# Performance work log

Hardware: AMD Instinct MI355X
Metric: run time of the kernel (lower is better)

## Reference

```python
import jax, jax.numpy as jnp
import numpy as np

H = 8  # number of heads


def setup_inputs() -> dict:
    key = jax.random.key(0)
    ks = jax.random.split(key, 7)
    B, L, D = 4, 2048, 512
    dh = D // H
    s = 1.0 / np.sqrt(D).astype(np.float32)
    return {
        "q": jax.random.normal(ks[0], (B, L, D), jnp.float32),
        "k": jax.random.normal(ks[1], (B, L, D), jnp.float32),
        "v": jax.random.normal(ks[2], (B, L, D), jnp.float32),
        "Wq": jax.random.normal(ks[3], (D, D), jnp.float32) * s,
        "Wk": jax.random.normal(ks[4], (D, D), jnp.float32) * s,
        "Wv": jax.random.normal(ks[5], (D, D), jnp.float32) * s,
        "E": jax.random.normal(ks[6], (L, dh), jnp.float32) * s,
    }


def _skew(QE):
    # QE: [B, H, L, L] -> pad one column on the left, reshape to [B,H,L+1,L],
    # drop the first row: the classic Music Transformer skewing trick.
    B, h, L, M = QE.shape
    padded = jnp.pad(QE, ((0, 0), (0, 0), (0, 0), (1, 0)))
    return padded.reshape(B, h, M + 1, L)[:, :, 1:, :]


def reference(q, k, v, Wq, Wk, Wv, E):
    B, L, D = q.shape
    dh = D // H

    def heads(x, W):
        return jnp.einsum('bld,de->ble', x, W).reshape(B, L, H, dh).transpose(0, 2, 1, 3)

    qh = heads(q, Wq)  # [B,H,L,dh]
    kh = heads(k, Wk)
    vh = heads(v, Wv)

    QE = jnp.einsum('bhld,md->bhlm', qh, E)      # [B,H,L,L]
    Srel = _skew(QE)                             # [B,H,L,L]
    QKt = jnp.einsum('bhld,bhmd->bhlm', qh, kh)  # [B,H,L,L]

    # NOTE: original divides AFTER softmax (faithful to source).
    attn = jax.nn.softmax(QKt + Srel, axis=-1) / float(np.sqrt(dh))
    out = jnp.einsum('bhlm,bhmd->bhld', attn, vh)
    return out.transpose(0, 2, 1, 3).reshape(B, L, D)
```

## Files before the change

kernel.cpp:

```cpp
#include <hip/hip_runtime.h>
#include <hip/hip_bf16.h>
#include <math.h>

typedef _Float16 f16;
typedef __attribute__((ext_vector_type(8))) _Float16 f16x8;
typedef __attribute__((ext_vector_type(4))) _Float16 f16x4;
typedef __attribute__((ext_vector_type(4))) float f32x4;

namespace {
constexpr int B = 4, L = 2048, D = 512, NH = 8, DH = 64;
}

__global__ __launch_bounds__(256)
void ecast_kernel(const float* __restrict__ E, f16* __restrict__ Ef) {
    int i4 = (blockIdx.x * 256 + threadIdx.x) * 4;
    float4 x = *(const float4*)(E + i4);
    *(f16x4*)(Ef + i4) = (f16x4){(f16)x.x, (f16)x.y, (f16)x.z, (f16)x.w};
}

__global__ __launch_bounds__(256)
void wtrans_kernel(const float* __restrict__ Wq, const float* __restrict__ Wk,
                   const float* __restrict__ Wv, f16* __restrict__ Wt) {
    __shared__ f16 Ws[64 * 65];
    const int sel = blockIdx.z;
    const float* W = (sel == 0) ? Wq : (sel == 1) ? Wk : Wv;
    f16* Wo = Wt + (size_t)sel * D * D;
    const int k0 = blockIdx.x * 64, n0 = blockIdx.y * 64;
    const int t = threadIdx.x;
#pragma unroll
    for (int i = 0; i < 16; ++i) {
        int idx = 256 * i + t;
        int r = idx >> 6, c = idx & 63;
        Ws[r * 65 + c] = (f16)W[(size_t)(k0 + r) * D + n0 + c];
    }
    __syncthreads();
    const int c = t >> 2, kseg = t & 3;
    f16x8 r0, r1;
#pragma unroll
    for (int j = 0; j < 8; ++j) r0[j] = Ws[(kseg * 16 + j) * 65 + c];
#pragma unroll
    for (int j = 0; j < 8; ++j) r1[j] = Ws[(kseg * 16 + 8 + j) * 65 + c];
    f16* o = Wo + (size_t)(n0 + c) * D + k0 + kseg * 16;
    *(f16x8*)o = r0;
    *(f16x8*)(o + 8) = r1;
}

__global__ __launch_bounds__(256, 4)
void proj_gemm(const float* __restrict__ q, const float* __restrict__ k,
               const float* __restrict__ v, const f16* __restrict__ Wt,
               f16* __restrict__ Qf, f16* __restrict__ Kf, f16* __restrict__ Vtf) {
    __shared__ f16 As[128 * 72];
    __shared__ f16 Bs[64 * 72];
    const int bx = blockIdx.x, by = blockIdx.y;
    const int sel = by >> 3, h = by & 7;
    const int m0 = bx * 128;
    const float* X = (sel == 0) ? q : (sel == 1) ? k : v;
    const f16* Bt = Wt + (size_t)sel * D * D + (size_t)h * 64 * D;
    const int t = threadIdx.x, wid = t >> 6, lane = t & 63;
    const int quad = lane >> 4, col = lane & 15;
    const int mw = wid * 32;

    f32x4 acc[2][4];
#pragma unroll
    for (int i = 0; i < 2; ++i)
#pragma unroll
        for (int j = 0; j < 4; ++j) acc[i][j] = (f32x4){0.f, 0.f, 0.f, 0.f};

    float4 xa[8];
    f16x8 breg[2];
    auto loadG = [&](int k0) {
#pragma unroll
        for (int i = 0; i < 8; ++i) {
            int idx = 256 * i + t;
            int r = idx >> 4, c4 = idx & 15;
            xa[i] = *(const float4*)(X + (size_t)(m0 + r) * D + k0 + c4 * 4);
        }
#pragma unroll
        for (int i = 0; i < 2; ++i) {
            int idx = 256 * i + t;
            int r = idx >> 3, ch = idx & 7;
            breg[i] = *(const f16x8*)(Bt + (size_t)r * D + k0 + ch * 8);
        }
    };
    auto storeL = [&]() {
#pragma unroll
        for (int i = 0; i < 8; ++i) {
            int idx = 256 * i + t;
            int r = idx >> 4, c4 = idx & 15;
            *(f16x4*)(As + r * 72 + c4 * 4) =
                (f16x4){(f16)xa[i].x, (f16)xa[i].y, (f16)xa[i].z, (f16)xa[i].w};
        }
#pragma unroll
        for (int i = 0; i < 2; ++i) {
            int idx = 256 * i + t;
            int r = idx >> 3, ch = idx & 7;
            *(f16x8*)(Bs + r * 72 + ch * 8) = breg[i];
        }
    };

    loadG(0);
    for (int k0 = 0; k0 < D; k0 += 64) {
        __syncthreads();
        storeL();
        __syncthreads();
        if (k0 + 64 < D) loadG(k0 + 64);
#pragma unroll
        for (int ks = 0; ks < 2; ++ks) {
            f16x8 af[2], bf[4];
#pragma unroll
            for (int mt = 0; mt < 2; ++mt)
                af[mt] = *(const f16x8*)(As + (mw + mt * 16 + col) * 72 + quad * 8 + ks * 32);
#pragma unroll
            for (int nt = 0; nt < 4; ++nt)
                bf[nt] = *(const f16x8*)(Bs + (nt * 16 + col) * 72 + quad * 8 + ks * 32);
#pragma unroll
            for (int mt = 0; mt < 2; ++mt)
#pragma unroll
                for (int nt = 0; nt < 4; ++nt)
                    acc[mt][nt] = __builtin_amdgcn_mfma_f32_16x16x32_f16(af[mt], bf[nt], acc[mt][nt], 0, 0, 0);
        }
    }

    if (sel < 2) {
        f16* Y = (sel == 0) ? Qf : Kf;
#pragma unroll
        for (int mt = 0; mt < 2; ++mt)
#pragma unroll
            for (int nt = 0; nt < 4; ++nt)
#pragma unroll
                for (int reg = 0; reg < 4; ++reg) {
                    int m = m0 + mw + mt * 16 + quad * 4 + reg;
                    int bb = m >> 11, l = m & 2047, d = nt * 16 + col;
                    Y[((size_t)(bb * NH + h) * L + l) * DH + d] = (f16)acc[mt][nt][reg];
                }
    } else {
        __syncthreads();
        f16* Cs = As;
#pragma unroll
        for (int mt = 0; mt < 2; ++mt)
#pragma unroll
            for (int nt = 0; nt < 4; ++nt)
#pragma unroll
                for (int reg = 0; reg < 4; ++reg) {
                    int d = nt * 16 + col;
                    int lc = mw + mt * 16 + quad * 4 + reg;
                    Cs[d * 136 + lc] = (f16)acc[mt][nt][reg];
                }
        __syncthreads();
        const int dd = t >> 2, seg = t & 3;
        const int bb = m0 >> 11, l0 = m0 & 2047;
        f16* Yv = Vtf + ((size_t)(bb * NH + h) * DH + dd) * L + l0 + seg * 32;
#pragma unroll
        for (int j = 0; j < 4; ++j)
            *(f16x8*)(Yv + j * 8) = *(const f16x8*)(Cs + dd * 136 + seg * 32 + j * 8);
    }
}

__global__ __launch_bounds__(256, 4)
void attn_kernel(const f16* __restrict__ Qf, const f16* __restrict__ Kf,
                 const f16* __restrict__ Vtf, const f16* __restrict__ Ef,
                 float* __restrict__ out) {
    __shared__ f16 KfS[64 * 72];
    __shared__ f16 VfS[64 * 72];
    __shared__ f16 Pbuf[4][16 * 72];

    const int t = threadIdx.x, wid = t >> 6, lane = t & 63;
    const int quad = lane >> 4, col = lane & 15;
    const int l0w = blockIdx.x * 64 + wid * 16;
    const int h = blockIdx.y, bb = blockIdx.z;
    const size_t head = (size_t)(bb * NH + h) * (size_t)(L * DH);
    const f16* qf = Qf + head;
    const f16* kf = Kf + head;
    const f16* vt = Vtf + head;
    f16* Pw = Pbuf[wid];

    f16x8 qF[2], qS[2];
    {
        const int m = l0w + col;
        const int mS = min(m + 1, L - 1);
#pragma unroll
        for (int ks = 0; ks < 2; ++ks) {
            const int off = quad * 8 + ks * 32;
            qF[ks] = *(const f16x8*)(qf + (size_t)m * DH + off);
            qS[ks] = *(const f16x8*)(qf + (size_t)mS * DH + off);
        }
    }

    f16x8 kreg[2], vreg[2];
    auto loadKV = [&](int c0) {
#pragma unroll
        for (int i = 0; i < 2; ++i) {
            int idx = 256 * i + t;
            int r = idx >> 3, ch = idx & 7;
            kreg[i] = *(const f16x8*)(kf + (size_t)(c0 + r) * DH + ch * 8);
            vreg[i] = *(const f16x8*)(vt + (size_t)r * L + c0 + ch * 8);
        }
    };

    f32x4 O[4];
#pragma unroll
    for (int i = 0; i < 4; ++i) O[i] = (f32x4){0.f, 0.f, 0.f, 0.f};
    float mrow[4] = {-1e30f, -1e30f, -1e30f, -1e30f};
    float srow[4] = {0.f, 0.f, 0.f, 0.f};

    loadKV(0);
    for (int c0 = 0; c0 < L; c0 += 64) {
        __syncthreads();
#pragma unroll
        for (int i = 0; i < 2; ++i) {
            int idx = 256 * i + t;
            int r = idx >> 3, ch = idx & 7;
            *(f16x8*)(KfS + r * 72 + ch * 8) = kreg[i];
            *(f16x8*)(VfS + r * 72 + ch * 8) = vreg[i];
        }
        __syncthreads();
        if (c0 + 64 < L) loadKV(c0 + 64);

        const int d0 = c0 - l0w;

        f32x4 S[4];
#pragma unroll
        for (int ns = 0; ns < 4; ++ns) {
            S[ns] = (f32x4){0.f, 0.f, 0.f, 0.f};
#pragma unroll
            for (int ks = 0; ks < 2; ++ks) {
                f16x8 bh = *(const f16x8*)(KfS + (ns * 16 + col) * 72 + quad * 8 + ks * 32);
                S[ns] = __builtin_amdgcn_mfma_f32_16x16x32_f16(qF[ks], bh, S[ns], 0, 0, 0);
            }
        }

        const bool doA = (d0 <= 15);
        const bool doB = (d0 >= -61);
#pragma unroll 1
        for (int pass = 0; pass < 2; ++pass) {
            if ((pass == 0 && !doA) || (pass == 1 && !doB)) continue;
            const int jbase = (pass == 0) ? (d0 + L - 16) : (d0 - 17);
            f32x4 G[5];
#pragma unroll
            for (int g = 0; g < 5; ++g) {
                int er = min(max(jbase + g * 16 + col, 0), L - 1);
                G[g] = (f32x4){0.f, 0.f, 0.f, 0.f};
                const size_t eb = (size_t)er * DH + quad * 8;
#pragma unroll
                for (int ks = 0; ks < 2; ++ks) {
                    f16x8 e8 = *(const f16x8*)(Ef + eb + ks * 32);
                    G[g] = __builtin_amdgcn_mfma_f32_16x16x32_f16(
                               (pass == 0) ? qF[ks] : qS[ks], e8, G[g], 0, 0, 0);
                }
            }
#pragma unroll
            for (int reg = 0; reg < 4; ++reg) {
                const int r  = quad * 4 + reg;
                const int jj = col - r + 15;
                const int src = quad * 16 + (jj & 15);
#pragma unroll
                for (int ns = 0; ns < 4; ++ns) {
                    float v0 = __shfl(G[ns][reg], src, 64);
                    float v1 = __shfl(G[ns + 1][reg], src, 64);
                    float val = (jj < 16) ? v0 : v1;
                    const int rel = d0 + ns * 16 + col - r;
                    const bool use = (pass == 0) ? (rel <= 0) : (rel >= 2);
                    if (use) S[ns][reg] += val;
                }
            }
        }

#pragma unroll
        for (int reg = 0; reg < 4; ++reg) {
            float tm = fmaxf(fmaxf(S[0][reg], S[1][reg]), fmaxf(S[2][reg], S[3][reg]));
#pragma unroll
            for (int msk = 1; msk < 16; msk <<= 1)
                tm = fmaxf(tm, __shfl_xor(tm, msk, 16));
            const float mnew  = fmaxf(mrow[reg], tm);
            const float alpha = __expf(mrow[reg] - mnew);
            float p[4], ps = 0.f;
#pragma unroll
            for (int ns = 0; ns < 4; ++ns) { p[ns] = __expf(S[ns][reg] - mnew); ps += p[ns]; }
#pragma unroll
            for (int msk = 1; msk < 16; msk <<= 1)
                ps += __shfl_xor(ps, msk, 16);
            srow[reg] = srow[reg] * alpha + ps;
            mrow[reg] = mnew;
            const int r = quad * 4 + reg;
#pragma unroll
            for (int ns = 0; ns < 4; ++ns) {
                O[ns][reg] *= alpha;
                Pw[r * 72 + ns * 16 + col] = (f16)p[ns];
            }
        }

        f16x8 pA[2];
        pA[0] = *(const f16x8*)(Pw + col * 72 + quad * 8);
        pA[1] = *(const f16x8*)(Pw + col * 72 + 32 + quad * 8);
#pragma unroll
        for (int ns = 0; ns < 4; ++ns) {
#pragma unroll
            for (int ks = 0; ks < 2; ++ks) {
                f16x8 v8 = *(const f16x8*)(VfS + (ns * 16 + col) * 72 + quad * 8 + ks * 32);
                O[ns] = __builtin_amdgcn_mfma_f32_16x16x32_f16(pA[ks], v8, O[ns], 0, 0, 0);
            }
        }
    }

#pragma unroll
    for (int reg = 0; reg < 4; ++reg) {
        const int l = l0w + quad * 4 + reg;
        const float inv = 1.0f / (srow[reg] * 8.0f);
        float* o = out + ((size_t)bb * L + l) * D + h * DH;
#pragma unroll
        for (int ns = 0; ns < 4; ++ns)
            o[ns * 16 + col] = O[ns][reg] * inv;
    }
}

extern "C" void kernel_launch(void* const* d_in, const int* in_sizes, int n_in,
                              void* d_out, int out_size, void* d_ws, size_t ws_size,
                              hipStream_t stream) {
    const float* q  = (const float*)d_in[0];
    const float* k  = (const float*)d_in[1];
    const float* v  = (const float*)d_in[2];
    const float* Wq = (const float*)d_in[3];
    const float* Wk = (const float*)d_in[4];
    const float* Wv = (const float*)d_in[5];
    const float* E  = (const float*)d_in[6];
    float* out = (float*)d_out;

    const size_t plane = (size_t)B * NH * L * DH;
    f16* Qf  = (f16*)d_ws;
    f16* Kfp = Qf + plane;
    f16* Vtf = Kfp + plane;
    f16* Wt  = Vtf + plane;
    f16* Ef  = Wt + (size_t)3 * D * D;

    ecast_kernel<<<L * DH / 1024, 256, 0, stream>>>(E, Ef);
    wtrans_kernel<<<dim3(8, 8, 3), 256, 0, stream>>>(Wq, Wk, Wv, Wt);
    proj_gemm<<<dim3(64, 24), 256, 0, stream>>>(q, k, v, Wt, Qf, Kfp, Vtf);
    attn_kernel<<<dim3(L / 64, NH, B), 256, 0, stream>>>(Qf, Kfp, Vtf, Ef, out);
}
```

Measured before the change: 354.8 us.

## Split attention over key range, swizzle LDS tiles, remap projection block order

Attention now splits the key dimension in two (flash-decoding style), writing unnormalized partial outputs and row max/sum stats that a new combine kernel merges. This doubles the number of workgroups (1024 to 2048) to fill more CUs. K/V shared tiles drop padding in favour of an XOR swizzle to avoid LDS bank conflicts. Projection GEMM blocks are remapped so that neighbouring blocks land on different XCDs. The split adds extra fp32 partial writes and reads plus a kernel launch, and it only runs when the workspace is large enough.

```diff
diff --git a/kernel.cpp b/kernel.cpp
--- a/kernel.cpp
+++ b/kernel.cpp
@@ -51,7 +51,9 @@
                f16* __restrict__ Qf, f16* __restrict__ Kf, f16* __restrict__ Vtf) {
     __shared__ f16 As[128 * 72];
     __shared__ f16 Bs[64 * 72];
-    const int bx = blockIdx.x, by = blockIdx.y;
+    const int flat = blockIdx.x;
+    const int wg = (flat & 7) * 192 + (flat >> 3);
+    const int by = wg % 24, bx = wg / 24;
     const int sel = by >> 3, h = by & 7;
     const int m0 = bx * 128;
     const float* X = (sel == 0) ? q : (sel == 1) ? k : v;
@@ -156,23 +158,30 @@
     }
 }
 
+template <int NS>
 __global__ __launch_bounds__(256, 4)
 void attn_kernel(const f16* __restrict__ Qf, const f16* __restrict__ Kf,
                  const f16* __restrict__ Vtf, const f16* __restrict__ Ef,
-                 float* __restrict__ out) {
-    __shared__ f16 KfS[64 * 72];
-    __shared__ f16 VfS[64 * 72];
-    __shared__ f16 Pbuf[4][16 * 72];
+                 float* __restrict__ out, float* __restrict__ Opart,
+                 float2* __restrict__ stats) {
+    __shared__ __align__(16) f16 KfS[64 * 64];
+    __shared__ __align__(16) f16 VfS[64 * 64];
+    __shared__ __align__(16) f16 Pbuf[4][16 * 72];
 
     const int t = threadIdx.x, wid = t >> 6, lane = t & 63;
     const int quad = lane >> 4, col = lane & 15;
     const int l0w = blockIdx.x * 64 + wid * 16;
-    const int h = blockIdx.y, bb = blockIdx.z;
+    const int h = blockIdx.y;
+    const int bz = blockIdx.z;
+    const int bb = (NS == 1) ? bz : (bz >> 1);
+    const int split = (NS == 1) ? 0 : (bz & 1);
+    const int cbeg = split * (L / NS), cend = cbeg + L / NS;
     const size_t head = (size_t)(bb * NH + h) * (size_t)(L * DH);
     const f16* qf = Qf + head;
     const f16* kf = Kf + head;
     const f16* vt = Vtf + head;
     f16* Pw = Pbuf[wid];
+    const int rsw = col & 7;
 
     f16x8 qF[2], qS[2];
     {
@@ -203,18 +212,19 @@
     float mrow[4] = {-1e30f, -1e30f, -1e30f, -1e30f};
     float srow[4] = {0.f, 0.f, 0.f, 0.f};
 
-    loadKV(0);
-    for (int c0 = 0; c0 < L; c0 += 64) {
+    loadKV(cbeg);
+    for (int c0 = cbeg; c0 < cend; c0 += 64) {
         __syncthreads();
 #pragma unroll
         for (int i = 0; i < 2; ++i) {
             int idx = 256 * i + t;
             int r = idx >> 3, ch = idx & 7;
-            *(f16x8*)(KfS + r * 72 + ch * 8) = kreg[i];
-            *(f16x8*)(VfS + r * 72 + ch * 8) = vreg[i];
-        }
-        __syncthreads();
-        if (c0 + 64 < L) loadKV(c0 + 64);
+            int sw = ((ch ^ (r & 7)) << 3);
+            *(f16x8*)(KfS + r * 64 + sw) = kreg[i];
+            *(f16x8*)(VfS + r * 64 + sw) = vreg[i];
+        }
+        __syncthreads();
+        if (c0 + 64 < cend) loadKV(c0 + 64);
 
         const int d0 = c0 - l0w;
 
@@ -224,7 +234,8 @@
             S[ns] = (f32x4){0.f, 0.f, 0.f, 0.f};
 #pragma unroll
             for (int ks = 0; ks < 2; ++ks) {
-                f16x8 bh = *(const f16x8*)(KfS + (ns * 16 + col) * 72 + quad * 8 + ks * 32);
+                f16x8 bh = *(const f16x8*)(KfS + (ns * 16 + col) * 64 +
+                                           (((quad + ks * 4) ^ rsw) << 3));
                 S[ns] = __builtin_amdgcn_mfma_f32_16x16x32_f16(qF[ks], bh, S[ns], 0, 0, 0);
             }
         }
@@ -296,21 +307,61 @@
         for (int ns = 0; ns < 4; ++ns) {
 #pragma unroll
             for (int ks = 0; ks < 2; ++ks) {
-                f16x8 v8 = *(const f16x8*)(VfS + (ns * 16 + col) * 72 + quad * 8 + ks * 32);
+                f16x8 v8 = *(const f16x8*)(VfS + (ns * 16 + col) * 64 +
+                                           (((quad + ks * 4) ^ rsw) << 3));
                 O[ns] = __builtin_amdgcn_mfma_f32_16x16x32_f16(pA[ks], v8, O[ns], 0, 0, 0);
             }
         }
     }
 
-#pragma unroll
-    for (int reg = 0; reg < 4; ++reg) {
-        const int l = l0w + quad * 4 + reg;
-        const float inv = 1.0f / (srow[reg] * 8.0f);
-        float* o = out + ((size_t)bb * L + l) * D + h * DH;
-#pragma unroll
-        for (int ns = 0; ns < 4; ++ns)
-            o[ns * 16 + col] = O[ns][reg] * inv;
-    }
+    if (NS == 1) {
+#pragma unroll
+        for (int reg = 0; reg < 4; ++reg) {
+            const int l = l0w + quad * 4 + reg;
+            const float inv = 1.0f / (srow[reg] * 8.0f);
+            float* o = out + ((size_t)bb * L + l) * D + h * DH;
+#pragma unroll
+            for (int ns = 0; ns < 4; ++ns)
+                o[ns * 16 + col] = O[ns][reg] * inv;
+        }
+    } else {
+#pragma unroll
+        for (int reg = 0; reg < 4; ++reg) {
+            const int l = l0w + quad * 4 + reg;
+            const size_t rowid = ((size_t)(split * B + bb) * NH + h) * L + l;
+            float* op = Opart + rowid * DH;
+#pragma unroll
+            for (int ns = 0; ns < 4; ++ns)
+                op[ns * 16 + col] = O[ns][reg];
+            if (col == 0) stats[rowid] = make_float2(mrow[reg], srow[reg]);
+        }
+    }
+}
+
+__global__ __launch_bounds__(256)
+void combine_kernel(const float* __restrict__ Opart, const float2* __restrict__ stats,
+                    float* __restrict__ out) {
+    constexpr size_t OPLANE = (size_t)B * NH * L * DH;
+    constexpr int SROWS = B * NH * L;
+    const int gid = blockIdx.x * 256 + threadIdx.x;
+    const int d4 = gid & 15;
+    const int row = gid >> 4;
+    const float2 s0 = stats[row];
+    const float2 s1 = stats[SROWS + row];
+    const float M = fmaxf(s0.x, s1.x);
+    const float w0 = __expf(s0.x - M), w1 = __expf(s1.x - M);
+    const float inv = 1.0f / ((w0 * s0.y + w1 * s1.y) * 8.0f);
+    const float4 o0 = *(const float4*)(Opart + (size_t)row * DH + d4 * 4);
+    const float4 o1 = *(const float4*)(Opart + OPLANE + (size_t)row * DH + d4 * 4);
+    const int l = row & (L - 1);
+    const int bh = row >> 11;
+    const int hh = bh & 7, bbb = bh >> 3;
+    float4 r;
+    r.x = (w0 * o0.x + w1 * o1.x) * inv;
+    r.y = (w0 * o0.y + w1 * o1.y) * inv;
+    r.z = (w0 * o0.z + w1 * o1.z) * inv;
+    r.w = (w0 * o0.w + w1 * o1.w) * inv;
+    *(float4*)(out + ((size_t)bbb * L + l) * D + hh * DH + d4 * 4) = r;
 }
 
 extern "C" void kernel_launch(void* const* d_in, const int* in_sizes, int n_in,
@@ -331,9 +382,22 @@
     f16* Vtf = Kfp + plane;
     f16* Wt  = Vtf + plane;
     f16* Ef  = Wt + (size_t)3 * D * D;
+    const size_t base_bytes = (3 * plane + 3 * (size_t)D * D + (size_t)L * DH) * sizeof(f16);
+    float*  Opart = (float*)((char*)d_ws + base_bytes);
+    float2* stats = (float2*)((char*)d_ws + base_bytes + 2 * plane * sizeof(float));
+    const size_t need = base_bytes + 2 * plane * sizeof(float)
+                        + (size_t)2 * B * NH * L * sizeof(float2);
+    const bool split2 = (ws_size >= need);
 
     ecast_kernel<<<L * DH / 1024, 256, 0, stream>>>(E, Ef);
     wtrans_kernel<<<dim3(8, 8, 3), 256, 0, stream>>>(Wq, Wk, Wv, Wt);
-    proj_gemm<<<dim3(64, 24), 256, 0, stream>>>(q, k, v, Wt, Qf, Kfp, Vtf);
-    attn_kernel<<<dim3(L / 64, NH, B), 256, 0, stream>>>(Qf, Kfp, Vtf, Ef, out);
-}
+    proj_gemm<<<dim3(1536), 256, 0, stream>>>(q, k, v, Wt, Qf, Kfp, Vtf);
+    if (split2) {
+        attn_kernel<2><<<dim3(L / 64, NH, B * 2), 256, 0, stream>>>(Qf, Kfp, Vtf, Ef,
+                                                                    out, Opart, stats);
+        combine_kernel<<<(B * NH * L * 16) / 256, 256, 0, stream>>>(Opart, stats, out);
+    } else {
+        attn_kernel<1><<<dim3(L / 64, NH, B), 256, 0, stream>>>(Qf, Kfp, Vtf, Ef,
+                                                                out, Opart, stats);
+    }
+}
```

After: 392.4 us. 1.11x slower.

## Precast inputs to fp16, remap projection blocks, and compute softmax row sums via MFMA

Applied to the files above, without the earlier changes.

Adds a separate kernel that casts q/k/v to fp16 once, so the projection GEMM reads half the bytes per tile. The GEMM now uses a flat grid with a swizzled block order to group tiles across XCDs. In attention, the per-row softmax sum is computed with an MFMA against a ones vector instead of shuffle reductions, the first two max-reduction steps use DPP, and s_setprio is raised around the MFMA sections. The cost is an extra kernel launch plus a full fp16 copy of the inputs written to and read back from memory, and the row sum is now taken over fp16-rounded probabilities.

```diff
diff --git a/kernel.cpp b/kernel.cpp
--- a/kernel.cpp
+++ b/kernel.cpp
@@ -9,6 +9,13 @@
 
 namespace {
 constexpr int B = 4, L = 2048, D = 512, NH = 8, DH = 64;
+}
+
+__device__ __forceinline__ float dpp_xor1(float x) {
+    return __int_as_float(__builtin_amdgcn_update_dpp(0, __float_as_int(x), 0xB1, 0xF, 0xF, true));
+}
+__device__ __forceinline__ float dpp_xor2(float x) {
+    return __int_as_float(__builtin_amdgcn_update_dpp(0, __float_as_int(x), 0x4E, 0xF, 0xF, true));
 }
 
 __global__ __launch_bounds__(256)
@@ -16,6 +23,17 @@
     int i4 = (blockIdx.x * 256 + threadIdx.x) * 4;
     float4 x = *(const float4*)(E + i4);
     *(f16x4*)(Ef + i4) = (f16x4){(f16)x.x, (f16)x.y, (f16)x.z, (f16)x.w};
+}
+
+__global__ __launch_bounds__(256)
+void xcast_kernel(const float* __restrict__ q, const float* __restrict__ k,
+                  const float* __restrict__ v, f16* __restrict__ Xf) {
+    const int sel = blockIdx.y;
+    const float* X = (sel == 0) ? q : (sel == 1) ? k : v;
+    const size_t i4 = ((size_t)blockIdx.x * 256 + threadIdx.x) * 4;
+    float4 x = *(const float4*)(X + i4);
+    *(f16x4*)(Xf + (size_t)sel * ((size_t)B * L * D) + i4) =
+        (f16x4){(f16)x.x, (f16)x.y, (f16)x.z, (f16)x.w};
 }
 
 __global__ __launch_bounds__(256)
@@ -46,15 +64,16 @@
 }
 
 __global__ __launch_bounds__(256, 4)
-void proj_gemm(const float* __restrict__ q, const float* __restrict__ k,
-               const float* __restrict__ v, const f16* __restrict__ Wt,
+void proj_gemm(const f16* __restrict__ Xf, const f16* __restrict__ Wt,
                f16* __restrict__ Qf, f16* __restrict__ Kf, f16* __restrict__ Vtf) {
     __shared__ f16 As[128 * 72];
     __shared__ f16 Bs[64 * 72];
-    const int bx = blockIdx.x, by = blockIdx.y;
+    const int flat = blockIdx.x;
+    const int wg = (flat & 7) * 192 + (flat >> 3);
+    const int by = wg % 24, bx = wg / 24;
     const int sel = by >> 3, h = by & 7;
     const int m0 = bx * 128;
-    const float* X = (sel == 0) ? q : (sel == 1) ? k : v;
+    const f16* X = Xf + (size_t)sel * ((size_t)B * L * D);
     const f16* Bt = Wt + (size_t)sel * D * D + (size_t)h * 64 * D;
     const int t = threadIdx.x, wid = t >> 6, lane = t & 63;
     const int quad = lane >> 4, col = lane & 15;
@@ -66,14 +85,14 @@
 #pragma unroll
         for (int j = 0; j < 4; ++j) acc[i][j] = (f32x4){0.f, 0.f, 0.f, 0.f};
 
-    float4 xa[8];
+    f16x8 xa[4];
     f16x8 breg[2];
     auto loadG = [&](int k0) {
 #pragma unroll
-        for (int i = 0; i < 8; ++i) {
-            int idx = 256 * i + t;
-            int r = idx >> 4, c4 = idx & 15;
-            xa[i] = *(const float4*)(X + (size_t)(m0 + r) * D + k0 + c4 * 4);
+        for (int i = 0; i < 4; ++i) {
+            int idx = 256 * i + t;
+            int r = idx >> 3, ch = idx & 7;
+            xa[i] = *(const f16x8*)(X + (size_t)(m0 + r) * D + k0 + ch * 8);
         }
 #pragma unroll
         for (int i = 0; i < 2; ++i) {
@@ -84,11 +103,10 @@
     };
     auto storeL = [&]() {
 #pragma unroll
-        for (int i = 0; i < 8; ++i) {
-            int idx = 256 * i + t;
-            int r = idx >> 4, c4 = idx & 15;
-            *(f16x4*)(As + r * 72 + c4 * 4) =
-                (f16x4){(f16)xa[i].x, (f16)xa[i].y, (f16)xa[i].z, (f16)xa[i].w};
+        for (int i = 0; i < 4; ++i) {
+            int idx = 256 * i + t;
+            int r = idx >> 3, ch = idx & 7;
+            *(f16x8*)(As + r * 72 + ch * 8) = xa[i];
         }
 #pragma unroll
         for (int i = 0; i < 2; ++i) {
@@ -174,6 +192,9 @@
     const f16* vt = Vtf + head;
     f16* Pw = Pbuf[wid];
 
+    const f16x8 ones8 = {(f16)1.f, (f16)1.f, (f16)1.f, (f16)1.f,
+                         (f16)1.f, (f16)1.f, (f16)1.f, (f16)1.f};
+
     f16x8 qF[2], qS[2];
     {
         const int m = l0w + col;
@@ -200,8 +221,8 @@
     f32x4 O[4];
 #pragma unroll
     for (int i = 0; i < 4; ++i) O[i] = (f32x4){0.f, 0.f, 0.f, 0.f};
+    f32x4 sacc = (f32x4){0.f, 0.f, 0.f, 0.f};
     float mrow[4] = {-1e30f, -1e30f, -1e30f, -1e30f};
-    float srow[4] = {0.f, 0.f, 0.f, 0.f};
 
     loadKV(0);
     for (int c0 = 0; c0 < L; c0 += 64) {
@@ -219,6 +240,7 @@
         const int d0 = c0 - l0w;
 
         f32x4 S[4];
+        __builtin_amdgcn_s_setprio(1);
 #pragma unroll
         for (int ns = 0; ns < 4; ++ns) {
             S[ns] = (f32x4){0.f, 0.f, 0.f, 0.f};
@@ -228,6 +250,7 @@
                 S[ns] = __builtin_amdgcn_mfma_f32_16x16x32_f16(qF[ks], bh, S[ns], 0, 0, 0);
             }
         }
+        __builtin_amdgcn_s_setprio(0);
 
         const bool doA = (d0 <= 15);
         const bool doB = (d0 >= -61);
@@ -268,30 +291,29 @@
 #pragma unroll
         for (int reg = 0; reg < 4; ++reg) {
             float tm = fmaxf(fmaxf(S[0][reg], S[1][reg]), fmaxf(S[2][reg], S[3][reg]));
-#pragma unroll
-            for (int msk = 1; msk < 16; msk <<= 1)
-                tm = fmaxf(tm, __shfl_xor(tm, msk, 16));
+            tm = fmaxf(tm, dpp_xor1(tm));
+            tm = fmaxf(tm, dpp_xor2(tm));
+            tm = fmaxf(tm, __shfl_xor(tm, 4, 16));
+            tm = fmaxf(tm, __shfl_xor(tm, 8, 16));
             const float mnew  = fmaxf(mrow[reg], tm);
             const float alpha = __expf(mrow[reg] - mnew);
-            float p[4], ps = 0.f;
-#pragma unroll
-            for (int ns = 0; ns < 4; ++ns) { p[ns] = __expf(S[ns][reg] - mnew); ps += p[ns]; }
-#pragma unroll
-            for (int msk = 1; msk < 16; msk <<= 1)
-                ps += __shfl_xor(ps, msk, 16);
-            srow[reg] = srow[reg] * alpha + ps;
             mrow[reg] = mnew;
+            sacc[reg] *= alpha;
             const int r = quad * 4 + reg;
 #pragma unroll
             for (int ns = 0; ns < 4; ++ns) {
+                float p = __expf(S[ns][reg] - mnew);
                 O[ns][reg] *= alpha;
-                Pw[r * 72 + ns * 16 + col] = (f16)p[ns];
+                Pw[r * 72 + ns * 16 + col] = (f16)p;
             }
         }
 
         f16x8 pA[2];
         pA[0] = *(const f16x8*)(Pw + col * 72 + quad * 8);
         pA[1] = *(const f16x8*)(Pw + col * 72 + 32 + quad * 8);
+        __builtin_amdgcn_s_setprio(1);
+        sacc = __builtin_amdgcn_mfma_f32_16x16x32_f16(pA[0], ones8, sacc, 0, 0, 0);
+        sacc = __builtin_amdgcn_mfma_f32_16x16x32_f16(pA[1], ones8, sacc, 0, 0, 0);
 #pragma unroll
         for (int ns = 0; ns < 4; ++ns) {
 #pragma unroll
@@ -300,12 +322,13 @@
                 O[ns] = __builtin_amdgcn_mfma_f32_16x16x32_f16(pA[ks], v8, O[ns], 0, 0, 0);
             }
         }
+        __builtin_amdgcn_s_setprio(0);
     }
 
 #pragma unroll
     for (int reg = 0; reg < 4; ++reg) {
         const int l = l0w + quad * 4 + reg;
-        const float inv = 1.0f / (srow[reg] * 8.0f);
+        const float inv = 1.0f / (sacc[reg] * 8.0f);
         float* o = out + ((size_t)bb * L + l) * D + h * DH;
 #pragma unroll
         for (int ns = 0; ns < 4; ++ns)
@@ -331,9 +354,11 @@
     f16* Vtf = Kfp + plane;
     f16* Wt  = Vtf + plane;
     f16* Ef  = Wt + (size_t)3 * D * D;
+    f16* Xf  = Ef + (size_t)L * DH;
 
     ecast_kernel<<<L * DH / 1024, 256, 0, stream>>>(E, Ef);
+    xcast_kernel<<<dim3((unsigned)(plane / 1024), 3), 256, 0, stream>>>(q, k, v, Xf);
     wtrans_kernel<<<dim3(8, 8, 3), 256, 0, stream>>>(Wq, Wk, Wv, Wt);
-    proj_gemm<<<dim3(64, 24), 256, 0, stream>>>(q, k, v, Wt, Qf, Kfp, Vtf);
+    proj_gemm<<<dim3(1536), 256, 0, stream>>>(Xf, Wt, Qf, Kfp, Vtf);
     attn_kernel<<<dim3(L / 64, NH, B), 256, 0, stream>>>(Qf, Kfp, Vtf, Ef, out);
 }
```

New measurement: 324.4 us. 1.09x faster.
